# Kernel optimization log

Measured on AMD Instinct MI355X. Metric: run time of the kernel, lower is better.

## Reference

```python
import jax, jax.numpy as jnp
import numpy as np

N = 100000
E = 1600000
IN_DIM = 64
HID = 64


def _glorot(key, shape):
    fan_in, fan_out = shape[0], shape[1]
    lim = np.sqrt(6.0 / (fan_in + fan_out))
    return jax.random.uniform(key, shape, jnp.float32, -lim, lim)


def setup_inputs() -> dict:
    key = jax.random.key(0)
    ks = jax.random.split(key, 14)
    x = jax.random.normal(ks[0], (N, IN_DIM), jnp.float32)
    edge_index = jax.random.randint(ks[1], (2, E), 0, N, jnp.int64)
    dims = [(IN_DIM, HID), (HID, HID), (HID, HID), (HID, 1)]
    inp = {"x": x, "edge_index": edge_index}
    for i, (di, do) in enumerate(dims, start=1):
        inp[f"Wself{i}"] = _glorot(ks[2 + 3 * (i - 1)], (di, do))
        inp[f"Wneigh{i}"] = _glorot(ks[3 + 3 * (i - 1)], (di, do))
        inp[f"b{i}"] = jnp.zeros((do,), jnp.float32)
    return inp


def _gn_block(h, src, dst, deg_inv, Wself, Wneigh, b, act):
    # gather -> scatter-add -> mean -> dense transform (GraphConv-style)
    msg = h[src]                                           # [E, d]
    agg = jax.ops.segment_sum(msg, dst, num_segments=N)    # [N, d]
    agg = agg * deg_inv                                    # mean aggregation
    out = h @ Wself + agg @ Wneigh + b
    return act(out)


def reference(x, edge_index, Wself1, Wneigh1, b1, Wself2, Wneigh2, b2,
              Wself3, Wneigh3, b3, Wself4, Wneigh4, b4):
    src, dst = edge_index[0], edge_index[1]
    deg = jax.ops.segment_sum(jnp.ones((E,), x.dtype), dst, num_segments=N)
    deg_inv = (1.0 / jnp.maximum(deg, 1.0))[:, None]       # [N, 1]
    relu = jax.nn.relu
    h = _gn_block(x, src, dst, deg_inv, Wself1, Wneigh1, b1, relu)
    h = _gn_block(h, src, dst, deg_inv, Wself2, Wneigh2, b2, relu)
    h = _gn_block(h, src, dst, deg_inv, Wself3, Wneigh3, b3, relu)
    h = _gn_block(h, src, dst, deg_inv, Wself4, Wneigh4, b4, lambda z: z)
    return jax.nn.sigmoid(h)                               # [N, 1]
```

## Files before the change

### kernel.cpp

```cpp
#include <hip/hip_runtime.h>
#include <hip/hip_bf16.h>
#include <math.h>


using bfrag = __attribute__((ext_vector_type(8))) short;
using ffrag = __attribute__((ext_vector_type(4))) float;

#define BKT_SHIFT 9
#define BKT_NODES (1 << BKT_SHIFT)
#define AGG_STRIDE 72

__device__ __forceinline__ int load_idx32(const int* __restrict__ ei32, int is64,
                                          long long pos) {
    return is64 ? ei32[2 * pos] : ei32[pos];
}

__device__ __forceinline__ unsigned short f2b_rne(float f) {
    union { float f; unsigned u; } c;
    c.f = f;
    unsigned r = c.u + 0x7FFFu + ((c.u >> 16) & 1u);
    return (unsigned short)(r >> 16);
}

__device__ __forceinline__ float b2f(unsigned short u) {
    union { unsigned u; float f; } c;
    c.u = ((unsigned)u) << 16;
    return c.f;
}

__global__ void bprep_init_kernel(
    const float* __restrict__ Ws1, const float* __restrict__ Wn1,
    const float* __restrict__ Ws2, const float* __restrict__ Wn2,
    const float* __restrict__ Ws3, const float* __restrict__ Wn3,
    unsigned short* __restrict__ bthi, unsigned short* __restrict__ btlo,
    const int* __restrict__ ei, int* __restrict__ bktc, int* __restrict__ flag) {
    if (blockIdx.x == 0) {
        bktc[threadIdx.x] = 0;
        if (threadIdx.x == 0) {
            int allz = 1;
            for (int i = 0; i < 32; ++i)
                if (ei[2 * i + 1] != 0) allz = 0;
            *flag = allz;
        }
    }
    int i = blockIdx.x * 256 + threadIdx.x;
    if (i >= 3 * 8192) return;
    int layer = i >> 13;
    int j = i & 8191;
    int n = j >> 7, k = j & 127;
    const float* Ws = layer == 0 ? Ws1 : (layer == 1 ? Ws2 : Ws3);
    const float* Wn = layer == 0 ? Wn1 : (layer == 1 ? Wn2 : Wn3);
    float v = (k < 64) ? Ws[k * 64 + n] : Wn[(k - 64) * 64 + n];
    unsigned short hi = f2b_rne(v);
    bthi[i] = hi;
    btlo[i] = f2b_rne(v - b2f(hi));
}

__global__ void split_x_kernel(const float4* __restrict__ in, ushort4* __restrict__ hi,
                               int n4) {
    int i = blockIdx.x * blockDim.x + threadIdx.x;
    if (i >= n4) return;
    float4 v = in[i];
    ushort4 h;
    h.x = f2b_rne(v.x); h.y = f2b_rne(v.y); h.z = f2b_rne(v.z); h.w = f2b_rne(v.w);
    hi[i] = h;
}

__global__ __launch_bounds__(256) void binA_kernel(
    const int* __restrict__ ei32, const int* __restrict__ flagp,
    int* __restrict__ bktCnt, unsigned* __restrict__ bins, int E, int nbkt,
    int cap, int chunksz) {
    __shared__ int cnt[256];
    __shared__ int base[256];
    int is64 = *flagp;
    int elo = blockIdx.x * chunksz;
    int ehi = min(E, elo + chunksz);
    if (elo >= E) return;
    for (int i = threadIdx.x; i < nbkt; i += 256) cnt[i] = 0;
    __syncthreads();
    for (int e = elo + (int)threadIdx.x; e < ehi; e += 256) {
        int dst = load_idx32(ei32, is64, (long long)E + e);
        atomicAdd(&cnt[dst >> BKT_SHIFT], 1);
    }
    __syncthreads();
    for (int i = threadIdx.x; i < nbkt; i += 256) {
        base[i] = atomicAdd(&bktCnt[i], cnt[i]);
        cnt[i] = 0;
    }
    __syncthreads();
    for (int e = elo + (int)threadIdx.x; e < ehi; e += 256) {
        int dst = load_idx32(ei32, is64, (long long)E + e);
        int src = load_idx32(ei32, is64, e);
        int b = dst >> BKT_SHIFT;
        int r = atomicAdd(&cnt[b], 1);
        bins[(size_t)b * cap + base[b] + r] =
            ((unsigned)(dst & (BKT_NODES - 1)) << 23) | (unsigned)src;
    }
}

__global__ __launch_bounds__(256) void bucketCSR_kernel(
    const int* __restrict__ bktCnt, const unsigned* __restrict__ bins,
    int* __restrict__ off, int* __restrict__ offe, int* __restrict__ col,
    float* __restrict__ dinv, int N, int cap) {
    __shared__ int deg[BKT_NODES];
    __shared__ int loc[BKT_NODES];
    __shared__ int ssum[256];
    int b = blockIdx.x;
    int lo = b << BKT_SHIFT;
    int n = min(BKT_NODES, N - lo);
    for (int i = threadIdx.x; i < BKT_NODES; i += 256) deg[i] = 0;
    __syncthreads();
    int cnt = bktCnt[b];
    const unsigned* bb = bins + (size_t)b * cap;
    for (int i = threadIdx.x; i < cnt; i += 256)
        atomicAdd(&deg[bb[i] >> 23], 1);
    __syncthreads();
    int t = threadIdx.x;
    int d0 = deg[2 * t], d1 = deg[2 * t + 1];
    int s = d0 + d1;
    ssum[t] = s;
    __syncthreads();
    for (int o = 1; o < 256; o <<= 1) {
        int v = (t >= o) ? ssum[t - o] : 0;
        __syncthreads();
        ssum[t] += v;
        __syncthreads();
    }
    int excl = ssum[t] - s;
    loc[2 * t] = excl;
    loc[2 * t + 1] = excl + d0;
    __syncthreads();
    int base = b * cap;
    for (int i = threadIdx.x; i < n; i += 256) {
        int d = deg[i];
        off[lo + i] = base + loc[i];
        offe[lo + i] = base + loc[i] + d;
        dinv[lo + i] = 1.0f / fmaxf((float)d, 1.0f);
    }
    __syncthreads();
    for (int i = threadIdx.x; i < cnt; i += 256) {
        unsigned p = bb[i];
        int pos = atomicAdd(&loc[p >> 23], 1);
        col[base + pos] = (int)(p & 0x7FFFFFu);
    }
}

__device__ __forceinline__ void gather_node(
    const unsigned short* __restrict__ Hhi, const int* __restrict__ off,
    const int* __restrict__ offe, const int* __restrict__ col,
    const float* __restrict__ dinv, unsigned short* __restrict__ aggRow,
    int n, int N, int g, int t16) {
    if (n >= N) {
        if (g == 0) {
            ushort4 z = {0, 0, 0, 0};
            *(ushort4*)&aggRow[t16 * 4] = z;
        }
        return;
    }
    int e = off[n], end = offe[n];
    float4 a0 = make_float4(0.f, 0.f, 0.f, 0.f);
    float4 a1 = make_float4(0.f, 0.f, 0.f, 0.f);
    float4 a2 = make_float4(0.f, 0.f, 0.f, 0.f);
    float4 a3 = make_float4(0.f, 0.f, 0.f, 0.f);
    for (; e + 16 <= end; e += 16) {
        int s0 = col[e + g];
        int s1 = col[e + 4 + g];
        int s2 = col[e + 8 + g];
        int s3 = col[e + 12 + g];
        ushort4 u0 = *(const ushort4*)&Hhi[(size_t)s0 * 64 + t16 * 4];
        ushort4 u1 = *(const ushort4*)&Hhi[(size_t)s1 * 64 + t16 * 4];
        ushort4 u2 = *(const ushort4*)&Hhi[(size_t)s2 * 64 + t16 * 4];
        ushort4 u3 = *(const ushort4*)&Hhi[(size_t)s3 * 64 + t16 * 4];
        a0.x += b2f(u0.x); a0.y += b2f(u0.y); a0.z += b2f(u0.z); a0.w += b2f(u0.w);
        a1.x += b2f(u1.x); a1.y += b2f(u1.y); a1.z += b2f(u1.z); a1.w += b2f(u1.w);
        a2.x += b2f(u2.x); a2.y += b2f(u2.y); a2.z += b2f(u2.z); a2.w += b2f(u2.w);
        a3.x += b2f(u3.x); a3.y += b2f(u3.y); a3.z += b2f(u3.z); a3.w += b2f(u3.w);
    }
    for (; e + 8 <= end; e += 8) {
        int s0 = col[e + g];
        int s1 = col[e + 4 + g];
        ushort4 u0 = *(const ushort4*)&Hhi[(size_t)s0 * 64 + t16 * 4];
        ushort4 u1 = *(const ushort4*)&Hhi[(size_t)s1 * 64 + t16 * 4];
        a0.x += b2f(u0.x); a0.y += b2f(u0.y); a0.z += b2f(u0.z); a0.w += b2f(u0.w);
        a1.x += b2f(u1.x); a1.y += b2f(u1.y); a1.z += b2f(u1.z); a1.w += b2f(u1.w);
    }
    for (; e < end; e += 4) {
        if (e + g < end) {
            int s0 = col[e + g];
            ushort4 u0 = *(const ushort4*)&Hhi[(size_t)s0 * 64 + t16 * 4];
            a2.x += b2f(u0.x); a2.y += b2f(u0.y); a2.z += b2f(u0.z); a2.w += b2f(u0.w);
        }
    }
    float4 acc;
    acc.x = (a0.x + a1.x) + (a2.x + a3.x);
    acc.y = (a0.y + a1.y) + (a2.y + a3.y);
    acc.z = (a0.z + a1.z) + (a2.z + a3.z);
    acc.w = (a0.w + a1.w) + (a2.w + a3.w);
#pragma unroll
    for (int msk = 16; msk <= 32; msk <<= 1) {
        acc.x += __shfl_xor(acc.x, msk, 64);
        acc.y += __shfl_xor(acc.y, msk, 64);
        acc.z += __shfl_xor(acc.z, msk, 64);
        acc.w += __shfl_xor(acc.w, msk, 64);
    }
    if (g == 0) {
        float di = dinv[n];
        ushort4 h;
        h.x = f2b_rne(acc.x * di);
        h.y = f2b_rne(acc.y * di);
        h.z = f2b_rne(acc.z * di);
        h.w = f2b_rne(acc.w * di);
        *(ushort4*)&aggRow[t16 * 4] = h;
    }
}

__global__ __launch_bounds__(256) void layer_fused_kernel(
    const unsigned short* __restrict__ Hhi, const int* __restrict__ off,
    const int* __restrict__ offe, const int* __restrict__ col,
    const float* __restrict__ dinv,
    const unsigned short* __restrict__ Bthi, const unsigned short* __restrict__ Btlo,
    const float* __restrict__ b, unsigned short* __restrict__ Dhi, int N) {
    __shared__ unsigned short aggL[16 * AGG_STRIDE];
    int wave = threadIdx.x >> 6;
    int lane = threadIdx.x & 63;
    int g = lane >> 4;
    int t16 = lane & 15;
    int n0 = blockIdx.x * 16;
#pragma unroll
    for (int i = 0; i < 4; ++i) {
        int li = wave * 4 + i;
        gather_node(Hhi, off, offe, col, dinv, aggL + li * AGG_STRIDE,
                    n0 + li, N, g, t16);
    }
    __syncthreads();
    int m = t16, quad = g;
    int nr = n0 + m;
    if (nr > N - 1) nr = N - 1;
    const unsigned short* hrow = Hhi + (size_t)nr * 64 + quad * 8;
    bfrag ah[4];
    ah[0] = *(const bfrag*)(hrow);
    ah[1] = *(const bfrag*)(hrow + 32);
    ah[2] = *(const bfrag*)&aggL[m * AGG_STRIDE + quad * 8];
    ah[3] = *(const bfrag*)&aggL[m * AGG_STRIDE + 32 + quad * 8];
    int oc = wave * 16 + m;
    float bl = b[oc];
    ffrag acc = {bl, bl, bl, bl};
#pragma unroll
    for (int c = 0; c < 4; ++c) {
        bfrag bh = *(const bfrag*)(Bthi + (size_t)oc * 128 + c * 32 + quad * 8);
        bfrag bw = *(const bfrag*)(Btlo + (size_t)oc * 128 + c * 32 + quad * 8);
        acc = __builtin_amdgcn_mfma_f32_16x16x32_bf16(ah[c], bh, acc, 0, 0, 0);
        acc = __builtin_amdgcn_mfma_f32_16x16x32_bf16(ah[c], bw, acc, 0, 0, 0);
    }
#pragma unroll
    for (int r = 0; r < 4; ++r) {
        int node = n0 + quad * 4 + r;
        if (node < N)
            Dhi[(size_t)node * 64 + oc] = f2b_rne(fmaxf(acc[r], 0.f));
    }
}

__global__ __launch_bounds__(256) void layer_fused_last_kernel(
    const unsigned short* __restrict__ Hhi, const int* __restrict__ off,
    const int* __restrict__ offe, const int* __restrict__ col,
    const float* __restrict__ dinv,
    const unsigned short* __restrict__ Bthi, const unsigned short* __restrict__ Btlo,
    const float* __restrict__ b, const float* __restrict__ Ws4,
    const float* __restrict__ Wn4, float* __restrict__ sbuf,
    float* __restrict__ gbuf, int N) {
    __shared__ unsigned short aggL[16 * AGG_STRIDE];
    __shared__ float sPart[4][16];
    __shared__ float gPart[4][16];
    int wave = threadIdx.x >> 6;
    int lane = threadIdx.x & 63;
    int g = lane >> 4;
    int t16 = lane & 15;
    int n0 = blockIdx.x * 16;
#pragma unroll
    for (int i = 0; i < 4; ++i) {
        int li = wave * 4 + i;
        gather_node(Hhi, off, offe, col, dinv, aggL + li * AGG_STRIDE,
                    n0 + li, N, g, t16);
    }
    __syncthreads();
    int m = t16, quad = g;
    int nr = n0 + m;
    if (nr > N - 1) nr = N - 1;
    const unsigned short* hrow = Hhi + (size_t)nr * 64 + quad * 8;
    bfrag ah[4];
    ah[0] = *(const bfrag*)(hrow);
    ah[1] = *(const bfrag*)(hrow + 32);
    ah[2] = *(const bfrag*)&aggL[m * AGG_STRIDE + quad * 8];
    ah[3] = *(const bfrag*)&aggL[m * AGG_STRIDE + 32 + quad * 8];
    int oc = wave * 16 + m;
    float bl = b[oc];
    ffrag acc = {bl, bl, bl, bl};
#pragma unroll
    for (int c = 0; c < 4; ++c) {
        bfrag bh = *(const bfrag*)(Bthi + (size_t)oc * 128 + c * 32 + quad * 8);
        bfrag bw = *(const bfrag*)(Btlo + (size_t)oc * 128 + c * 32 + quad * 8);
        acc = __builtin_amdgcn_mfma_f32_16x16x32_bf16(ah[c], bh, acc, 0, 0, 0);
        acc = __builtin_amdgcn_mfma_f32_16x16x32_bf16(ah[c], bw, acc, 0, 0, 0);
    }
    float w4s = Ws4[oc], w4n = Wn4[oc];
#pragma unroll
    for (int r = 0; r < 4; ++r) {
        float v = fmaxf(acc[r], 0.f);
        float ps = v * w4s;
        float pg = v * w4n;
#pragma unroll
        for (int mask = 1; mask <= 8; mask <<= 1) {
            ps += __shfl_xor(ps, mask, 64);
            pg += __shfl_xor(pg, mask, 64);
        }
        if (m == 0) {
            sPart[wave][quad * 4 + r] = ps;
            gPart[wave][quad * 4 + r] = pg;
        }
    }
    __syncthreads();
    if (threadIdx.x < 16) {
        int node = n0 + threadIdx.x;
        if (node < N) {
            float s = sPart[0][threadIdx.x] + sPart[1][threadIdx.x] +
                      sPart[2][threadIdx.x] + sPart[3][threadIdx.x];
            float gg = gPart[0][threadIdx.x] + gPart[1][threadIdx.x] +
                       gPart[2][threadIdx.x] + gPart[3][threadIdx.x];
            sbuf[node] = s;
            gbuf[node] = gg;
        }
    }
}

__global__ void final_kernel(const float* __restrict__ s, const float* __restrict__ dinv,
                             const float* __restrict__ g, const int* __restrict__ off,
                             const int* __restrict__ offe, const int* __restrict__ col,
                             const float* __restrict__ b4, float* __restrict__ out, int N) {
    int n = blockIdx.x * blockDim.x + threadIdx.x;
    if (n >= N) return;
    float a = 0.f;
    int e = off[n], end = offe[n];
    for (; e < end; ++e) a += g[col[e]];
    float z = s[n] + dinv[n] * a + b4[0];
    out[n] = 1.0f / (1.0f + expf(-z));
}

static inline int cdiv(long long a, long long b) { return (int)((a + b - 1) / b); }

extern "C" void kernel_launch(void* const* d_in, const int* in_sizes, int n_in,
                              void* d_out, int out_size, void* d_ws, size_t ws_size,
                              hipStream_t stream) {
    const float* x   = (const float*)d_in[0];
    const int*   ei  = (const int*)d_in[1];
    const float* Ws1 = (const float*)d_in[2];
    const float* Wn1 = (const float*)d_in[3];
    const float* b1  = (const float*)d_in[4];
    const float* Ws2 = (const float*)d_in[5];
    const float* Wn2 = (const float*)d_in[6];
    const float* b2  = (const float*)d_in[7];
    const float* Ws3 = (const float*)d_in[8];
    const float* Wn3 = (const float*)d_in[9];
    const float* b3  = (const float*)d_in[10];
    const float* Ws4 = (const float*)d_in[11];
    const float* Wn4 = (const float*)d_in[12];
    const float* b4  = (const float*)d_in[13];
    float* out = (float*)d_out;

    const int N = in_sizes[0] / 64;
    const int E = in_sizes[1] / 2;

    const int nbkt = cdiv(N, BKT_NODES);
    const int cap  = E / nbkt + E / nbkt / 8 + 64;

    unsigned* bins = (unsigned*)d_ws;
    int* col = (int*)(bins + (size_t)nbkt * cap);
    unsigned short* HhiA = (unsigned short*)(col + (size_t)nbkt * cap);
    unsigned short* HhiB = HhiA + (size_t)N * 64;
    unsigned short* Bth  = HhiB + (size_t)N * 64;
    unsigned short* Btl  = Bth + 3 * 8192;
    float* dinv = (float*)(Btl + 3 * 8192);
    float* sbuf = dinv + N;
    float* gbuf = sbuf + N;
    int*   off  = (int*)(gbuf + N);
    int*   offe = off + N;
    int*   bktc = offe + N;
    int*   flag = bktc + 256;

    const int BT = 256;
    const int gridN  = cdiv(N, BT);
    const int gridL  = cdiv(N, 16);
    const int binBlocks = 512;
    const int chunksz = cdiv(E, binBlocks);

    bprep_init_kernel<<<96, BT, 0, stream>>>(Ws1, Wn1, Ws2, Wn2, Ws3, Wn3,
                                             Bth, Btl, ei, bktc, flag);
    split_x_kernel<<<cdiv((long long)N * 16, BT), BT, 0, stream>>>(
        (const float4*)x, (ushort4*)HhiA, N * 16);

    binA_kernel<<<binBlocks, BT, 0, stream>>>(ei, flag, bktc, bins, E, nbkt, cap, chunksz);
    bucketCSR_kernel<<<nbkt, BT, 0, stream>>>(bktc, bins, off, offe, col, dinv, N, cap);

    layer_fused_kernel<<<gridL, BT, 0, stream>>>(HhiA, off, offe, col, dinv,
                                                 Bth, Btl, b1, HhiB, N);
    layer_fused_kernel<<<gridL, BT, 0, stream>>>(HhiB, off, offe, col, dinv,
                                                 Bth + 8192, Btl + 8192, b2, HhiA, N);
    layer_fused_last_kernel<<<gridL, BT, 0, stream>>>(HhiA, off, offe, col, dinv,
                                                      Bth + 16384, Btl + 16384, b3,
                                                      Ws4, Wn4, sbuf, gbuf, N);

    final_kernel<<<gridN, BT, 0, stream>>>(sbuf, dinv, gbuf, off, offe, col, b4, out, N);
}
```

Measured before the change: 400.0 us.

## Assign one node per 16-lane group in gather, removing cross-group shuffle reduction

The gather is restructured so that each 16-lane quarter-wave owns a whole destination node and walks all of its edges, instead of four groups splitting one node's edges and combining them with xor shuffles. Each wave now processes four nodes concurrently rather than four nodes in sequence. This removes the shuffle reduction and the serial per-node loop. The edge tail is handled by a branch-free, clamped, masked unrolled loop of seven loads. The risk is load imbalance between the four nodes in a wave, since degrees vary, plus extra wasted loads in the masked tail.

```diff
diff --git a/kernel.cpp b/kernel.cpp
--- a/kernel.cpp
+++ b/kernel.cpp
@@ -145,50 +145,59 @@
     }
 }
 
-__device__ __forceinline__ void gather_node(
+__device__ __forceinline__ void acc4(float4& a, ushort4 u) {
+    a.x += b2f(u.x); a.y += b2f(u.y); a.z += b2f(u.z); a.w += b2f(u.w);
+}
+
+__device__ __forceinline__ void fma4(float4& a, float m, ushort4 u) {
+    a.x = fmaf(m, b2f(u.x), a.x);
+    a.y = fmaf(m, b2f(u.y), a.y);
+    a.z = fmaf(m, b2f(u.z), a.z);
+    a.w = fmaf(m, b2f(u.w), a.w);
+}
+
+__device__ __forceinline__ void gather_node_v3(
     const unsigned short* __restrict__ Hhi, const int* __restrict__ off,
     const int* __restrict__ offe, const int* __restrict__ col,
     const float* __restrict__ dinv, unsigned short* __restrict__ aggRow,
-    int n, int N, int g, int t16) {
+    int n, int N, int t16) {
     if (n >= N) {
-        if (g == 0) {
-            ushort4 z = {0, 0, 0, 0};
-            *(ushort4*)&aggRow[t16 * 4] = z;
-        }
+        ushort4 z = make_ushort4(0, 0, 0, 0);
+        *(ushort4*)&aggRow[t16 * 4] = z;
         return;
     }
     int e = off[n], end = offe[n];
     float4 a0 = make_float4(0.f, 0.f, 0.f, 0.f);
-    float4 a1 = make_float4(0.f, 0.f, 0.f, 0.f);
-    float4 a2 = make_float4(0.f, 0.f, 0.f, 0.f);
-    float4 a3 = make_float4(0.f, 0.f, 0.f, 0.f);
-    for (; e + 16 <= end; e += 16) {
-        int s0 = col[e + g];
-        int s1 = col[e + 4 + g];
-        int s2 = col[e + 8 + g];
-        int s3 = col[e + 12 + g];
-        ushort4 u0 = *(const ushort4*)&Hhi[(size_t)s0 * 64 + t16 * 4];
-        ushort4 u1 = *(const ushort4*)&Hhi[(size_t)s1 * 64 + t16 * 4];
-        ushort4 u2 = *(const ushort4*)&Hhi[(size_t)s2 * 64 + t16 * 4];
-        ushort4 u3 = *(const ushort4*)&Hhi[(size_t)s3 * 64 + t16 * 4];
-        a0.x += b2f(u0.x); a0.y += b2f(u0.y); a0.z += b2f(u0.z); a0.w += b2f(u0.w);
-        a1.x += b2f(u1.x); a1.y += b2f(u1.y); a1.z += b2f(u1.z); a1.w += b2f(u1.w);
-        a2.x += b2f(u2.x); a2.y += b2f(u2.y); a2.z += b2f(u2.z); a2.w += b2f(u2.w);
-        a3.x += b2f(u3.x); a3.y += b2f(u3.y); a3.z += b2f(u3.z); a3.w += b2f(u3.w);
-    }
+    float4 a1 = a0, a2 = a0, a3 = a0;
+    const unsigned short* __restrict__ Hq = Hhi + t16 * 4;
     for (; e + 8 <= end; e += 8) {
-        int s0 = col[e + g];
-        int s1 = col[e + 4 + g];
-        ushort4 u0 = *(const ushort4*)&Hhi[(size_t)s0 * 64 + t16 * 4];
-        ushort4 u1 = *(const ushort4*)&Hhi[(size_t)s1 * 64 + t16 * 4];
-        a0.x += b2f(u0.x); a0.y += b2f(u0.y); a0.z += b2f(u0.z); a0.w += b2f(u0.w);
-        a1.x += b2f(u1.x); a1.y += b2f(u1.y); a1.z += b2f(u1.z); a1.w += b2f(u1.w);
-    }
-    for (; e < end; e += 4) {
-        if (e + g < end) {
-            int s0 = col[e + g];
-            ushort4 u0 = *(const ushort4*)&Hhi[(size_t)s0 * 64 + t16 * 4];
-            a2.x += b2f(u0.x); a2.y += b2f(u0.y); a2.z += b2f(u0.z); a2.w += b2f(u0.w);
+        int s0 = col[e + 0], s1 = col[e + 1], s2 = col[e + 2], s3 = col[e + 3];
+        int s4 = col[e + 4], s5 = col[e + 5], s6 = col[e + 6], s7 = col[e + 7];
+        ushort4 u0 = *(const ushort4*)&Hq[(size_t)s0 * 64];
+        ushort4 u1 = *(const ushort4*)&Hq[(size_t)s1 * 64];
+        ushort4 u2 = *(const ushort4*)&Hq[(size_t)s2 * 64];
+        ushort4 u3 = *(const ushort4*)&Hq[(size_t)s3 * 64];
+        ushort4 u4 = *(const ushort4*)&Hq[(size_t)s4 * 64];
+        ushort4 u5 = *(const ushort4*)&Hq[(size_t)s5 * 64];
+        ushort4 u6 = *(const ushort4*)&Hq[(size_t)s6 * 64];
+        ushort4 u7 = *(const ushort4*)&Hq[(size_t)s7 * 64];
+        acc4(a0, u0); acc4(a1, u1); acc4(a2, u2); acc4(a3, u3);
+        acc4(a0, u4); acc4(a1, u5); acc4(a2, u6); acc4(a3, u7);
+    }
+    int rem = end - e;
+    if (rem > 0) {
+        int last = end - 1;
+#pragma unroll
+        for (int j = 0; j < 7; ++j) {
+            int idx = e + j;
+            int cl = idx < last ? idx : last;
+            int s = col[cl];
+            ushort4 u = *(const ushort4*)&Hq[(size_t)s * 64];
+            float m = (j < rem) ? 1.0f : 0.0f;
+            if ((j & 3) == 0) fma4(a0, m, u);
+            else if ((j & 3) == 1) fma4(a1, m, u);
+            else if ((j & 3) == 2) fma4(a2, m, u);
+            else fma4(a3, m, u);
         }
     }
     float4 acc;
@@ -196,22 +205,13 @@
     acc.y = (a0.y + a1.y) + (a2.y + a3.y);
     acc.z = (a0.z + a1.z) + (a2.z + a3.z);
     acc.w = (a0.w + a1.w) + (a2.w + a3.w);
-#pragma unroll
-    for (int msk = 16; msk <= 32; msk <<= 1) {
-        acc.x += __shfl_xor(acc.x, msk, 64);
-        acc.y += __shfl_xor(acc.y, msk, 64);
-        acc.z += __shfl_xor(acc.z, msk, 64);
-        acc.w += __shfl_xor(acc.w, msk, 64);
-    }
-    if (g == 0) {
-        float di = dinv[n];
-        ushort4 h;
-        h.x = f2b_rne(acc.x * di);
-        h.y = f2b_rne(acc.y * di);
-        h.z = f2b_rne(acc.z * di);
-        h.w = f2b_rne(acc.w * di);
-        *(ushort4*)&aggRow[t16 * 4] = h;
-    }
+    float di = dinv[n];
+    ushort4 h;
+    h.x = f2b_rne(acc.x * di);
+    h.y = f2b_rne(acc.y * di);
+    h.z = f2b_rne(acc.z * di);
+    h.w = f2b_rne(acc.w * di);
+    *(ushort4*)&aggRow[t16 * 4] = h;
 }
 
 __global__ __launch_bounds__(256) void layer_fused_kernel(
@@ -226,12 +226,9 @@
     int g = lane >> 4;
     int t16 = lane & 15;
     int n0 = blockIdx.x * 16;
-#pragma unroll
-    for (int i = 0; i < 4; ++i) {
-        int li = wave * 4 + i;
-        gather_node(Hhi, off, offe, col, dinv, aggL + li * AGG_STRIDE,
-                    n0 + li, N, g, t16);
-    }
+    int li = wave * 4 + g;
+    gather_node_v3(Hhi, off, offe, col, dinv, aggL + li * AGG_STRIDE,
+                   n0 + li, N, t16);
     __syncthreads();
     int m = t16, quad = g;
     int nr = n0 + m;
@@ -276,12 +273,9 @@
     int g = lane >> 4;
     int t16 = lane & 15;
     int n0 = blockIdx.x * 16;
-#pragma unroll
-    for (int i = 0; i < 4; ++i) {
-        int li = wave * 4 + i;
-        gather_node(Hhi, off, offe, col, dinv, aggL + li * AGG_STRIDE,
-                    n0 + li, N, g, t16);
-    }
+    int li = wave * 4 + g;
+    gather_node_v3(Hhi, off, offe, col, dinv, aggL + li * AGG_STRIDE,
+                   n0 + li, N, t16);
     __syncthreads();
     int m = t16, quad = g;
     int nr = n0 + m;
```

Result: faster. 361.3 us (-9.7%).
